# Kernel tuning notes

Measured on AMD Instinct MI355X. Metric: run time of the kernel, lower is better.

Reference implementation:

```python
import jax, jax.numpy as jnp
import numpy as np

ALPHA = 1.0
INF = 1e4  # larger than any possible distance in a 256x256 image


def _row_dist_to_zero(x):
    """1D distance along last axis to nearest zero pixel. x: [..., W] (0/1)."""
    W = x.shape[-1]
    idx = jnp.arange(W, dtype=jnp.float32)
    is0 = x == 0
    # nearest zero at-or-before each position
    last0 = jax.lax.cummax(jnp.where(is0, idx, -1.0), axis=x.ndim - 1)
    fwd = jnp.where(last0 >= 0, idx - last0, INF)
    # nearest zero at-or-after each position (suffix max of -idx)
    neg_next0 = jax.lax.cummax(jnp.where(is0, -idx, -INF), axis=x.ndim - 1, reverse=True)
    bwd = jnp.where(neg_next0 > -INF, (-neg_next0) - idx, INF)
    return jnp.minimum(fwd, bwd)


def _edt_2d(target):
    """Exact Euclidean distance transform per [B,C] map: distance from nonzero
    pixels to nearest zero pixel (matches scipy.ndimage.distance_transform_edt)."""
    B, C, H, W = target.shape
    g = _row_dist_to_zero(target)            # [B,C,H,W] distance along width
    g2 = g * g
    i = jnp.arange(H, dtype=jnp.float32)
    dk2 = (i[:, None] - i[None, :]) ** 2     # [H(out), H(k)]
    # dt2[b,c,i,w] = min_k g2[b,c,k,w] + (i-k)^2
    d2 = jnp.min(g2[:, :, None, :, :] + dk2[None, None, :, :, None], axis=3)
    return jnp.sqrt(d2)


def _distance_map(target):
    dist = _edt_2d(target)
    dmax = jnp.max(dist, axis=(-2, -1), keepdims=True)
    return dist / (dmax + 1e-7)


def setup_inputs() -> dict:
    key = jax.random.key(0)
    k1, k2 = jax.random.split(key)
    pred = jax.random.normal(k1, (8, 1, 256, 256), dtype=jnp.float32)
    target = jax.random.randint(k2, (8, 1, 256, 256), 0, 2).astype(jnp.float32)
    return {"pred": pred, "target": target}


def reference(pred, target):
    dist_map = _distance_map(target)
    weight_map = 1.0 + ALPHA * dist_map
    # numerically stable BCE with logits, reduction='none'
    bce = jnp.maximum(pred, 0.0) - pred * target + jnp.log1p(jnp.exp(-jnp.abs(pred)))
    return jnp.mean(weight_map * bce)
```

## Files before the change

### kernel.cpp

```cpp
#include <hip/hip_runtime.h>
#include <math.h>

#define BATCH 8
#define H 256
#define W 256
#define NPIX (BATCH * H * W)
#define NBLK2 512

__device__ __forceinline__ float bce_logits(float p, float t) {
    return fmaxf(p, 0.0f) - p * t + log1pf(expf(-fabsf(p)));
}

__global__ void __launch_bounds__(256) row_edt(const float* __restrict__ target,
                                               float* __restrict__ g2) {
    __shared__ unsigned long long mlds[4][4];
    const int tid = threadIdx.x;
    const int v = tid >> 6, l = tid & 63;
    const float* imgr = target + (size_t)blockIdx.x * 4 * W;

    #pragma unroll
    for (int j = 0; j < 4; ++j) {
        float t = imgr[j * W + tid];
        unsigned long long m = __ballot(t == 0.0f);
        if (l == 0) mlds[j][v] = m;
    }
    __syncthreads();

    const int p = tid;
    #pragma unroll
    for (int j = 0; j < 4; ++j) {
        unsigned long long mw[4] = {mlds[j][0], mlds[j][1], mlds[j][2], mlds[j][3]};
        int best = 1 << 20;
        #pragma unroll
        for (int w = 0; w < 4; ++w) {
            const int rel = p - (w << 6);
            const unsigned long long m = mw[w];
            unsigned long long mlo = (rel < 0)  ? 0ull
                                   : (rel >= 63) ? m : (m & ((2ull << rel) - 1ull));
            unsigned long long mhi = (rel <= 0) ? m
                                   : (rel > 63)  ? 0ull : (m & (~0ull << rel));
            if (mlo) best = min(best, rel - (63 - __builtin_clzll(mlo)));
            if (mhi) best = min(best, __builtin_ctzll(mhi) - rel);
        }
        float d = (best > 255) ? 1e4f : (float)best;
        g2[(size_t)blockIdx.x * 4 * W + j * W + tid] = d * d;
    }
}

__global__ void __launch_bounds__(256) envelope_bce(
        const float* __restrict__ g2, const float* __restrict__ pred,
        const float* __restrict__ target,
        float* __restrict__ pmx, float* __restrict__ psb, float* __restrict__ psdb) {
    __shared__ float red[3][4];
    const int tid = threadIdx.x;
    const int wv = tid >> 6, l = tid & 63;
    const int b  = blockIdx.x >> 6;
    const int cs = (blockIdx.x >> 4) & 3;
    const int rs = blockIdx.x & 15;
    const int c  = (cs << 6) + l;
    const int i0 = (rs << 4) + (wv << 2);

    const float* pp = pred   + ((size_t)(b * H + i0)) * W + c;
    const float* tp = target + ((size_t)(b * H + i0)) * W + c;
    float p0 = pp[0], p1 = pp[W], p2 = pp[2 * W], p3 = pp[3 * W];
    float t0 = tp[0], t1 = tp[W], t2 = tp[2 * W], t3 = tp[3 * W];

    const float* gcol = g2 + (size_t)b * H * W + c;

    float acc0 = 3.0e38f, acc1 = 3.0e38f, acc2 = 3.0e38f, acc3 = 3.0e38f;
    int kd = i0 + 1, ku = i0 + 2;
    float fd0 = (float)(i0 - kd), fu0 = (float)(ku - i0);
    for (;;) {
        if (kd >= 0) {
            float g = gcol[(size_t)kd * W];
            acc0 = fminf(acc0, fmaf(fd0, fd0, g));
            float fd1 = fd0 + 1.0f, fd2 = fd0 + 2.0f, fd3 = fd0 + 3.0f;
            acc1 = fminf(acc1, fmaf(fd1, fd1, g));
            acc2 = fminf(acc2, fmaf(fd2, fd2, g));
            acc3 = fminf(acc3, fmaf(fd3, fd3, g));
        }
        if (ku <= 255) {
            float g = gcol[(size_t)ku * W];
            float fu1 = fu0 - 1.0f, fu2 = fu0 - 2.0f, fu3 = fu0 - 3.0f;
            acc0 = fminf(acc0, fmaf(fu0, fu0, g));
            acc1 = fminf(acc1, fmaf(fu1, fu1, g));
            acc2 = fminf(acc2, fmaf(fu2, fu2, g));
            acc3 = fminf(acc3, fmaf(fu3, fu3, g));
        }
        --kd; ++ku; fd0 += 1.0f; fu0 += 1.0f;
        float maxacc = fmaxf(fmaxf(acc0, acc1), fmaxf(acc2, acc3));
        float dn = (float)(i0 - kd);
        float up = (float)(ku - (i0 + 3));
        bool alive = (kd >= 0 && dn * dn <= maxacc) || (ku <= 255 && up * up <= maxacc);
        if (!__any(alive)) break;
    }

    float mx = fmaxf(fmaxf(acc0, acc1), fmaxf(acc2, acc3));
    float b0 = bce_logits(p0, t0), b1 = bce_logits(p1, t1);
    float b2 = bce_logits(p2, t2), b3 = bce_logits(p3, t3);
    float sb  = (b0 + b1) + (b2 + b3);
    float sdb = (sqrtf(acc0) * b0 + sqrtf(acc1) * b1)
              + (sqrtf(acc2) * b2 + sqrtf(acc3) * b3);

    #pragma unroll
    for (int o = 32; o > 0; o >>= 1) {
        mx  = fmaxf(mx, __shfl_down(mx, o, 64));
        sb  += __shfl_down(sb, o, 64);
        sdb += __shfl_down(sdb, o, 64);
    }
    if (l == 0) { red[0][wv] = mx; red[1][wv] = sb; red[2][wv] = sdb; }
    __syncthreads();
    if (tid == 0) {
        pmx [blockIdx.x] = fmaxf(fmaxf(red[0][0], red[0][1]), fmaxf(red[0][2], red[0][3]));
        psb [blockIdx.x] = (red[1][0] + red[1][1]) + (red[1][2] + red[1][3]);
        psdb[blockIdx.x] = (red[2][0] + red[2][1]) + (red[2][2] + red[2][3]);
    }
}

__global__ void final_reduce(const float* __restrict__ pmx, const float* __restrict__ psb,
                             const float* __restrict__ psdb, float* __restrict__ out) {
    const int tid = threadIdx.x;
    const int img = tid >> 5, j = tid & 31;
    const int e0 = (img << 6) + j, e1 = e0 + 32;
    float mx  = fmaxf(pmx[e0], pmx[e1]);
    float sb  = psb[e0] + psb[e1];
    float sdb = psdb[e0] + psdb[e1];
    #pragma unroll
    for (int o = 16; o > 0; o >>= 1) {
        mx  = fmaxf(mx, __shfl_down(mx, o, 32));
        sb  += __shfl_down(sb, o, 32);
        sdb += __shfl_down(sdb, o, 32);
    }
    __shared__ float cimg[8], simg[8];
    if (j == 0) {
        cimg[img] = sdb / (sqrtf(mx) + 1e-7f);
        simg[img] = sb;
    }
    __syncthreads();
    if (tid == 0) {
        float tot = 0.0f;
        #pragma unroll
        for (int i = 0; i < 8; ++i) tot += simg[i] + cimg[i];
        out[0] = tot * (1.0f / (float)NPIX);
    }
}

extern "C" void kernel_launch(void* const* d_in, const int* in_sizes, int n_in,
                              void* d_out, int out_size, void* d_ws, size_t ws_size,
                              hipStream_t stream) {
    const float* pred   = (const float*)d_in[0];
    const float* target = (const float*)d_in[1];

    float* g2   = (float*)d_ws;
    float* pmx  = (float*)((char*)d_ws + (size_t)NPIX * sizeof(float));
    float* psb  = pmx + NBLK2;
    float* psdb = psb + NBLK2;

    row_edt<<<BATCH * 64, 256, 0, stream>>>(target, g2);
    envelope_bce<<<NBLK2, 256, 0, stream>>>(g2, pred, target, pmx, psb, psdb);
    final_reduce<<<1, 256, 0, stream>>>(pmx, psb, psdb, (float*)d_out);
}
```

Measured before the change: 67.38 us.

## Halve rows per thread in envelope kernel and unroll initial search steps

Each thread in the column-envelope/BCE kernel now handles 2 rows instead of 4, doubling the block count to 1024 and adjusting the final reduction to match. The first 10 steps of the outward k-search are unrolled branchlessly with clamped loads, and the early-exit check moves to the loop head. This aims to raise parallelism and hide load latency in the common short-search case. The cost is less reuse of each loaded g2 value across output rows and more redundant loads and partial sums.

Result: faster. 65.34 us (-3.0%).

```diff
diff --git a/kernel.cpp b/kernel.cpp
--- a/kernel.cpp
+++ b/kernel.cpp
@@ -5,7 +5,7 @@
 #define H 256
 #define W 256
 #define NPIX (BATCH * H * W)
-#define NBLK2 512
+#define NBLK2 1024
 
 __device__ __forceinline__ float bce_logits(float p, float t) {
     return fmaxf(p, 0.0f) - p * t + log1pf(expf(-fabsf(p)));
@@ -54,53 +54,62 @@
     __shared__ float red[3][4];
     const int tid = threadIdx.x;
     const int wv = tid >> 6, l = tid & 63;
-    const int b  = blockIdx.x >> 6;
-    const int cs = (blockIdx.x >> 4) & 3;
-    const int rs = blockIdx.x & 15;
+    const int b  = blockIdx.x >> 7;
+    const int cs = (blockIdx.x >> 5) & 3;
+    const int rs = blockIdx.x & 31;
     const int c  = (cs << 6) + l;
-    const int i0 = (rs << 4) + (wv << 2);
+    const int i0 = (rs << 3) + (wv << 1);
 
-    const float* pp = pred   + ((size_t)(b * H + i0)) * W + c;
-    const float* tp = target + ((size_t)(b * H + i0)) * W + c;
-    float p0 = pp[0], p1 = pp[W], p2 = pp[2 * W], p3 = pp[3 * W];
-    float t0 = tp[0], t1 = tp[W], t2 = tp[2 * W], t3 = tp[3 * W];
+    const size_t po = ((size_t)(b * H + i0)) * W + c;
+    float p0 = pred[po], p1 = pred[po + W];
+    float t0 = target[po], t1 = target[po + W];
 
     const float* gcol = g2 + (size_t)b * H * W + c;
 
-    float acc0 = 3.0e38f, acc1 = 3.0e38f, acc2 = 3.0e38f, acc3 = 3.0e38f;
-    int kd = i0 + 1, ku = i0 + 2;
-    float fd0 = (float)(i0 - kd), fu0 = (float)(ku - i0);
+    float acc0 = 3.0e38f, acc1 = 3.0e38f;
+    const int P = 10;
+    #pragma unroll
+    for (int s = 0; s < P; ++s) {
+        const int kd = i0 + 1 - s;
+        const int ku = i0 + 2 + s;
+        float gd = gcol[(size_t)max(kd, 0) * W];
+        float gu = gcol[(size_t)min(ku, 255) * W];
+        if (kd < 0)   gd = 3.0e38f;
+        if (ku > 255) gu = 3.0e38f;
+        const float ed0 = (float)(s - 1), ed1 = (float)s;
+        const float eu0 = (float)(s + 2), eu1 = (float)(s + 1);
+        acc0 = fminf(acc0, fminf(fmaf(ed0, ed0, gd), fmaf(eu0, eu0, gu)));
+        acc1 = fminf(acc1, fminf(fmaf(ed1, ed1, gd), fmaf(eu1, eu1, gu)));
+    }
+
+    int kd = i0 + 1 - P, ku = i0 + 2 + P;
+    float fd0 = (float)(i0 - kd);
+    float fu0 = (float)(ku - i0);
     for (;;) {
+        float maxacc = fmaxf(acc0, acc1);
+        float dn = (float)(i0 - kd);
+        float up = (float)(ku - (i0 + 1));
+        bool alive = (kd >= 0 && dn * dn <= maxacc) || (ku <= 255 && up * up <= maxacc);
+        if (!__any(alive)) break;
         if (kd >= 0) {
             float g = gcol[(size_t)kd * W];
             acc0 = fminf(acc0, fmaf(fd0, fd0, g));
-            float fd1 = fd0 + 1.0f, fd2 = fd0 + 2.0f, fd3 = fd0 + 3.0f;
+            float fd1 = fd0 + 1.0f;
             acc1 = fminf(acc1, fmaf(fd1, fd1, g));
-            acc2 = fminf(acc2, fmaf(fd2, fd2, g));
-            acc3 = fminf(acc3, fmaf(fd3, fd3, g));
         }
         if (ku <= 255) {
             float g = gcol[(size_t)ku * W];
-            float fu1 = fu0 - 1.0f, fu2 = fu0 - 2.0f, fu3 = fu0 - 3.0f;
+            float fu1 = fu0 - 1.0f;
             acc0 = fminf(acc0, fmaf(fu0, fu0, g));
             acc1 = fminf(acc1, fmaf(fu1, fu1, g));
-            acc2 = fminf(acc2, fmaf(fu2, fu2, g));
-            acc3 = fminf(acc3, fmaf(fu3, fu3, g));
         }
         --kd; ++ku; fd0 += 1.0f; fu0 += 1.0f;
-        float maxacc = fmaxf(fmaxf(acc0, acc1), fmaxf(acc2, acc3));
-        float dn = (float)(i0 - kd);
-        float up = (float)(ku - (i0 + 3));
-        bool alive = (kd >= 0 && dn * dn <= maxacc) || (ku <= 255 && up * up <= maxacc);
-        if (!__any(alive)) break;
     }
 
-    float mx = fmaxf(fmaxf(acc0, acc1), fmaxf(acc2, acc3));
+    float mx = fmaxf(acc0, acc1);
     float b0 = bce_logits(p0, t0), b1 = bce_logits(p1, t1);
-    float b2 = bce_logits(p2, t2), b3 = bce_logits(p3, t3);
-    float sb  = (b0 + b1) + (b2 + b3);
-    float sdb = (sqrtf(acc0) * b0 + sqrtf(acc1) * b1)
-              + (sqrtf(acc2) * b2 + sqrtf(acc3) * b3);
+    float sb  = b0 + b1;
+    float sdb = sqrtf(acc0) * b0 + sqrtf(acc1) * b1;
 
     #pragma unroll
     for (int o = 32; o > 0; o >>= 1) {
@@ -121,10 +130,14 @@
                              const float* __restrict__ psdb, float* __restrict__ out) {
     const int tid = threadIdx.x;
     const int img = tid >> 5, j = tid & 31;
-    const int e0 = (img << 6) + j, e1 = e0 + 32;
-    float mx  = fmaxf(pmx[e0], pmx[e1]);
-    float sb  = psb[e0] + psb[e1];
-    float sdb = psdb[e0] + psdb[e1];
+    float mx = 0.0f, sb = 0.0f, sdb = 0.0f;
+    #pragma unroll
+    for (int q = 0; q < 4; ++q) {
+        const int e = (img << 7) + j + (q << 5);
+        mx  = fmaxf(mx, pmx[e]);
+        sb  += psb[e];
+        sdb += psdb[e];
+    }
     #pragma unroll
     for (int o = 16; o > 0; o >>= 1) {
         mx  = fmaxf(mx, __shfl_down(mx, o, 32));
```
